# Performance work log

Hardware: AMD Instinct MI355X
Metric: run time of the kernel (lower is better)

Reference implementation:

```python
import jax, jax.numpy as jnp
import numpy as np

D_MODEL = 512; N_HEADS = 8; D_HIDDEN = 512
STACK_DEPTH = 48; STACK_WIDTH = 128; D_FF = 2048; D_SS = 128
SEQ = 512; BATCH = 16
EP = 1e-4; MAX_ITER = 100


def nonsat(x):
    # fixed-point iteration y_ = (2y^3/3 + x)/(y^2+1); torch detaches y each step,
    # so grads flow only through x in the final step. Loop runs on stopped values.
    xs = jax.lax.stop_gradient(x)
    step = lambda y: (2.0 * y ** 3 / 3.0 + xs) / (y * y + 1.0)
    def cond(s):
        y, y_, i = s
        return jnp.logical_and(jnp.mean(jnp.abs(y_ - y)) > EP, i <= MAX_ITER)
    def body(s):
        y, y_, i = s
        return (y_, step(y_), i + 1)
    y_last, _, _ = jax.lax.while_loop(cond, body, (xs, step(xs), jnp.int32(0)))
    return (2.0 * y_last ** 3 / 3.0 + x) / (y_last * y_last + 1.0)


def layer_norm(x, g, b, eps=1e-5):
    m = jnp.mean(x, axis=-1, keepdims=True)
    v = jnp.mean((x - m) ** 2, axis=-1, keepdims=True)
    return (x - m) / jnp.sqrt(v + eps) * g + b


def mha(x, k_mask, wi, bi, wo, bo):
    # x: (S,B,E), torch nn.MultiheadAttention with combined in_proj, causal mask
    S, B, E = x.shape
    H = N_HEADS; hd = E // H
    qkv = x @ wi.T + bi
    q, k, v = jnp.split(qkv, 3, axis=-1)
    to_heads = lambda t: t.reshape(S, B, H, hd).transpose(1, 2, 0, 3)  # (B,H,S,hd)
    q = to_heads(q) * (hd ** -0.5)
    k = to_heads(k); v = to_heads(v)
    scores = jnp.einsum('bhqd,bhkd->bhqk', q, k)
    causal = jnp.triu(jnp.full((S, S), -jnp.inf, dtype=x.dtype), 1)
    scores = scores + causal
    scores = jnp.where(k_mask[:, None, None, :], -jnp.inf, scores)
    a = jax.nn.softmax(scores, axis=-1)
    o = jnp.einsum('bhqk,bhkd->bhqd', a, v).transpose(2, 0, 1, 3).reshape(S, B, E)
    return o @ wo.T + bo


def setup_inputs() -> dict:
    key = jax.random.key(0)
    ks = iter(jax.random.split(key, 32))
    E = D_MODEL
    def w(shape, fan_in):
        return (jax.random.normal(next(ks), shape, jnp.float32) / np.sqrt(fan_in)).astype(jnp.float32)
    inp = {
        'x_in': jax.random.normal(next(ks), (SEQ, BATCH, E), jnp.float32),
        'hidden_prev': jax.random.normal(next(ks), (BATCH, SEQ, D_HIDDEN), jnp.float32),
        'stack_prev': jax.random.normal(next(ks), (BATCH, SEQ, STACK_DEPTH, STACK_WIDTH), jnp.float32),
        'k_mask': jnp.zeros((BATCH, SEQ), dtype=bool),
        'in_proj_w': w((3 * E, E), E), 'in_proj_b': jnp.zeros((3 * E,), jnp.float32),
        'out_proj_w': w((E, E), E), 'out_proj_b': jnp.zeros((E,), jnp.float32),
        'ln1_g': jnp.ones((E,), jnp.float32), 'ln1_b': jnp.zeros((E,), jnp.float32),
        'ln2_g': jnp.ones((E,), jnp.float32), 'ln2_b': jnp.zeros((E,), jnp.float32),
        'ff_w1': w((D_FF, E), E), 'ff_b1': jnp.zeros((D_FF,), jnp.float32),
        'ff_w2': w((E, D_FF), D_FF), 'ff_b2': jnp.zeros((E,), jnp.float32),
        'W_w': w((D_HIDDEN, E), E), 'W_b': jnp.zeros((D_HIDDEN,), jnp.float32),
        'R_w': w((D_HIDDEN, D_HIDDEN), D_HIDDEN), 'R_b': jnp.zeros((D_HIDDEN,), jnp.float32),
        'P_w': w((D_HIDDEN, STACK_WIDTH), STACK_WIDTH), 'P_b': jnp.zeros((D_HIDDEN,), jnp.float32),
        'V_w': w((D_SS, E + D_HIDDEN), E + D_HIDDEN),
        'U_w': w((E, D_SS), D_SS),
        'A_w': w((3, D_HIDDEN), D_HIDDEN), 'A_b': jnp.zeros((3,), jnp.float32),
        'D_w': w((STACK_WIDTH, D_HIDDEN), D_HIDDEN), 'D_b': jnp.zeros((STACK_WIDTH,), jnp.float32),
    }
    return inp


def reference(x_in, hidden_prev, stack_prev, k_mask,
              in_proj_w, in_proj_b, out_proj_w, out_proj_b,
              ln1_g, ln1_b, ln2_g, ln2_b,
              ff_w1, ff_b1, ff_w2, ff_b2,
              W_w, W_b, R_w, R_b, P_w, P_b,
              V_w, U_w, A_w, A_b, D_w, D_b):
    # sublayer 1: pre-norm residual multihead self-attention
    x = x_in + mha(layer_norm(x_in, ln1_g, ln1_b), k_mask,
                   in_proj_w, in_proj_b, out_proj_w, out_proj_b)
    # stack-augmented memory update
    stack_x = stack_prev[:, :, 0, :]                       # (B,S,W) stack top
    xb = x.transpose(1, 0, 2)                              # (B,S,E)
    hidden = xb @ W_w.T + W_b + hidden_prev @ R_w.T + R_b + stack_x @ P_w.T + P_b
    hidden = nonsat(hidden)                                # (B,S,Dh)
    vx = jnp.concatenate([x, hidden.transpose(1, 0, 2)], axis=-1)  # (S,B,E+Dh)
    y = jax.nn.softmax(vx @ V_w.T, axis=-1) @ U_w.T        # (S,B,E)
    x = 0.5 * (x + y)
    stack_inp = nonsat(hidden @ D_w.T + D_b)[:, :, None, :]        # (B,S,1,W)
    controls = jax.nn.softmax(hidden @ A_w.T + A_b, axis=-1)       # (B,S,3)
    a_push = controls[:, :, 0, None, None]
    a_pop = controls[:, :, 1, None, None]
    a_noop = controls[:, :, 2, None, None]
    zeros_bot = jnp.zeros_like(stack_prev[:, :, :1])
    stack_down = jnp.concatenate([stack_prev[:, :, 1:], zeros_bot], axis=2)
    stack_up = jnp.concatenate([stack_inp, stack_prev[:, :, :-1]], axis=2)
    stack = a_noop * stack_prev + a_push * stack_up + a_pop * stack_down
    # sublayer 2: pre-norm residual position-wise FFN
    h = layer_norm(x, ln2_g, ln2_b)
    x = x + (jax.nn.relu(h @ ff_w1.T + ff_b1) @ ff_w2.T + ff_b2)
    return (x, hidden, stack)
```

## Files before the change

### kernel.cpp

```cpp
#include <hip/hip_runtime.h>
#include <stdint.h>

typedef unsigned short u16;
typedef short short8 __attribute__((ext_vector_type(8)));
typedef float f32x4 __attribute__((ext_vector_type(4)));

__device__ __forceinline__ u16 f2b(float f) {
    uint32_t x = __float_as_uint(f);
    uint32_t r = x + 0x7fffu + ((x >> 16) & 1u);
    return (u16)(r >> 16);
}

__device__ __forceinline__ float nonsat_f(float x) {
    float y = x;
#pragma unroll
    for (int t = 0; t < 14; ++t) {
        const float y2 = y * y;
        y = (0.66666667f * y2 * y + x) / (y2 + 1.f);
    }
    return y;
}

__device__ __forceinline__ void gl2lds16(const u16* g, u16* l) {
    __builtin_amdgcn_global_load_lds(
        (const __attribute__((address_space(1))) unsigned int*)g,
        (__attribute__((address_space(3))) unsigned int*)l, 16, 0, 0);
}

template <int MT, int MODE, bool RELU>
__global__ __launch_bounds__(256) void gemm_k(
    const u16* __restrict__ A, int lda,
    const u16* __restrict__ B, int ldb,
    const float* __restrict__ bias,
    int M, int N, int K,
    u16* __restrict__ out_b, float* __restrict__ out_f,
    const float* __restrict__ res_f, u16* __restrict__ out_b2)
{
    constexpr int MI = MT / 64;
    constexpr int WI = MT / 32;
    const int tn = blockIdx.x, tm = blockIdx.y;
    const int tid = threadIdx.x;
    const int wave = tid >> 6, lane = tid & 63;
    const int quad = lane >> 4, mm = lane & 15;
    const int wr = (wave >> 1) * (MT / 2), wc = (wave & 1) * 64;

    __shared__ __align__(16) u16 As[MT * 32];
    __shared__ __align__(16) u16 Bs[128 * 32];

    const f32x4 vzero = {0.f, 0.f, 0.f, 0.f};
    f32x4 acc[WI][4];
#pragma unroll
    for (int i = 0; i < WI; i++)
#pragma unroll
        for (int j = 0; j < 4; j++) acc[i][j] = vzero;

    const int lr = tid >> 2;
    const int lc = (tid & 3) * 8;
    const u16* ag[MI];
#pragma unroll
    for (int h = 0; h < MI; h++)
        ag[h] = A + (size_t)(tm * MT + lr + h * 64) * lda + lc;
    const u16* bg0 = B + (size_t)(tn * 128 + lr) * ldb + lc;
    const u16* bg1 = B + (size_t)(tn * 128 + lr + 64) * ldb + lc;
    u16* asl[MI];
#pragma unroll
    for (int h = 0; h < MI; h++) asl[h] = As + h * 2048 + wave * 512;
    u16* bsl0 = Bs + wave * 512;
    u16* bsl1 = Bs + 2048 + wave * 512;

    for (int kt = 0; kt < K; kt += 32) {
        __syncthreads();
#pragma unroll
        for (int h = 0; h < MI; h++) gl2lds16(ag[h] + kt, asl[h]);
        gl2lds16(bg0 + kt, bsl0);
        gl2lds16(bg1 + kt, bsl1);
        asm volatile("s_waitcnt vmcnt(0)" ::: "memory");
        __syncthreads();
        short8 af[WI], bfr[4];
#pragma unroll
        for (int i = 0; i < WI; i++) af[i] = *(const short8*)(As + (wr + i * 16 + mm) * 32 + quad * 8);
#pragma unroll
        for (int j = 0; j < 4; j++) bfr[j] = *(const short8*)(Bs + (wc + j * 16 + mm) * 32 + quad * 8);
#pragma unroll
        for (int i = 0; i < WI; i++)
#pragma unroll
            for (int j = 0; j < 4; j++)
                acc[i][j] = __builtin_amdgcn_mfma_f32_16x16x32_bf16(af[i], bfr[j], acc[i][j], 0, 0, 0);
    }

#pragma unroll
    for (int j = 0; j < 4; j++) {
        const int colg = tn * 128 + wc + j * 16 + mm;
        const float bv = bias ? bias[colg] : 0.f;
#pragma unroll
        for (int i = 0; i < WI; i++) {
#pragma unroll
            for (int r = 0; r < 4; r++) {
                const int rowg = tm * MT + wr + i * 16 + quad * 4 + r;
                float v = acc[i][j][r] + bv;
                const size_t off = (size_t)rowg * N + colg;
                if constexpr (MODE == 0) {
                    if (RELU) v = fmaxf(v, 0.f);
                    out_b[off] = f2b(v);
                } else if constexpr (MODE == 1) {
                    out_f[off] = v;
                } else if constexpr (MODE == 2) {
                    out_f[off] += v;
                } else if constexpr (MODE == 3) {
                    v += res_f[off];
                    out_f[off] = v;
                    const u16 hb = f2b(v);
                    out_b[off] = hb;
                    out_b2[((size_t)(rowg & 15) * 512 + (rowg >> 4)) * 512 + colg] = hb;
                } else if constexpr (MODE == 4) {
                    v = 0.5f * (v + res_f[off]);
                    out_f[off] = v;
                } else if constexpr (MODE == 5) {
                    v += res_f[off];
                    out_f[off] = v;
                } else if constexpr (MODE == 6) {
                    v = nonsat_f(v + res_f[off]);
                    out_f[off] = v;
                    out_b[off] = f2b(v);
                } else {
                    v = nonsat_f(v);
                    out_f[off] = v;
                }
            }
        }
    }
}

struct CvtArgs {
    const float* s[12];
    unsigned cum[13];
};

__global__ __launch_bounds__(256) void cvt_k(CvtArgs a, u16* __restrict__ arena)
{
    const unsigned t = (blockIdx.x * 256u + threadIdx.x) * 8u;
    if (t >= a.cum[12]) return;
    int g = 0;
#pragma unroll
    for (int i = 1; i < 12; i++)
        if (t >= a.cum[i]) g = i;
    const unsigned e = t - a.cum[g];
    const float* src = (g == 11) ? (a.s[11] + (size_t)(e >> 7) * 6144 + (e & 127))
                                 : (a.s[g] + e);
    float4 u0 = *(const float4*)src;
    float4 u1 = *(const float4*)(src + 4);
    __align__(16) u16 o[8] = {f2b(u0.x), f2b(u0.y), f2b(u0.z), f2b(u0.w),
                              f2b(u1.x), f2b(u1.y), f2b(u1.z), f2b(u1.w)};
    *(int4*)(arena + t) = *(const int4*)o;
}

__global__ __launch_bounds__(64) void attn_k(const u16* __restrict__ QKV, u16* __restrict__ O)
{
    const int qt = blockIdx.x;
    const int bh = blockIdx.y;
    const int b = bh >> 3, h = bh & 7;
    const int lane = threadIdx.x;
    const int quad = lane >> 4, mm = lane & 15;
    const int cbase = h * 64;
    const float NEGINF = -3.0e38f;

    __shared__ __align__(16) u16 Pl[64 * 72];
    __shared__ __align__(16) u16 Vl[64 * 72];

    short8 qf[4][2];
#pragma unroll
    for (int rt = 0; rt < 4; ++rt) {
        const int s = qt * 64 + rt * 16 + mm;
        const u16* p = QKV + ((size_t)s * 16 + b) * 1536 + cbase + quad * 8;
        qf[rt][0] = *(const short8*)(p);
        qf[rt][1] = *(const short8*)(p + 32);
    }

    const f32x4 vzero = {0.f, 0.f, 0.f, 0.f};
    f32x4 of[4][4];
#pragma unroll
    for (int i = 0; i < 4; i++)
#pragma unroll
        for (int j = 0; j < 4; j++) of[i][j] = vzero;
    float mrow[4][4], lrow[4][4];
#pragma unroll
    for (int i = 0; i < 4; i++)
#pragma unroll
        for (int r = 0; r < 4; r++) { mrow[i][r] = NEGINF; lrow[i][r] = 0.f; }

    for (int kt = 0; kt <= qt; ++kt) {
        short8 kf[4][2];
#pragma unroll
        for (int nt = 0; nt < 4; ++nt) {
            const int kk = kt * 64 + nt * 16 + mm;
            const u16* p = QKV + ((size_t)kk * 16 + b) * 1536 + 512 + cbase + quad * 8;
            kf[nt][0] = *(const short8*)(p);
            kf[nt][1] = *(const short8*)(p + 32);
        }
        f32x4 sf[4][4];
#pragma unroll
        for (int i = 0; i < 4; i++)
#pragma unroll
            for (int j = 0; j < 4; j++) sf[i][j] = vzero;
#pragma unroll
        for (int i = 0; i < 4; i++)
#pragma unroll
            for (int j = 0; j < 4; j++) {
                sf[i][j] = __builtin_amdgcn_mfma_f32_16x16x32_bf16(qf[i][0], kf[j][0], sf[i][j], 0, 0, 0);
                sf[i][j] = __builtin_amdgcn_mfma_f32_16x16x32_bf16(qf[i][1], kf[j][1], sf[i][j], 0, 0, 0);
            }
        {
            const int kk = lane >> 3, c8 = (lane & 7) * 8;
#pragma unroll
            for (int it = 0; it < 8; ++it) {
                const int key = kt * 64 + it * 8 + kk;
                int4 v = *(const int4*)(QKV + ((size_t)key * 16 + b) * 1536 + 1024 + cbase + c8);
                *(int4*)(Vl + (it * 8 + kk) * 72 + c8) = v;
            }
        }
        const bool diag = (kt == qt);
#pragma unroll
        for (int i = 0; i < 4; i++)
#pragma unroll
            for (int j = 0; j < 4; j++)
#pragma unroll
                for (int r = 0; r < 4; r++) {
                    float v = sf[i][j][r] * 0.125f;
                    if (diag) {
                        const int q = i * 16 + quad * 4 + r;
                        const int k = j * 16 + mm;
                        if (k > q) v = NEGINF;
                    }
                    sf[i][j][r] = v;
                }
#pragma unroll
        for (int i = 0; i < 4; i++) {
#pragma unroll
            for (int r = 0; r < 4; r++) {
                float mx = fmaxf(fmaxf(sf[i][0][r], sf[i][1][r]), fmaxf(sf[i][2][r], sf[i][3][r]));
                mx = fmaxf(mx, __shfl_xor(mx, 1));
                mx = fmaxf(mx, __shfl_xor(mx, 2));
                mx = fmaxf(mx, __shfl_xor(mx, 4));
                mx = fmaxf(mx, __shfl_xor(mx, 8));
                const float mnew = fmaxf(mrow[i][r], mx);
                const float alpha = __expf(mrow[i][r] - mnew);
                mrow[i][r] = mnew;
                float psum = 0.f;
#pragma unroll
                for (int j = 0; j < 4; j++) {
                    float p = __expf(sf[i][j][r] - mnew);
                    sf[i][j][r] = p;
                    psum += p;
                }
                psum += __shfl_xor(psum, 1);
                psum += __shfl_xor(psum, 2);
                psum += __shfl_xor(psum, 4);
                psum += __shfl_xor(psum, 8);
                lrow[i][r] = lrow[i][r] * alpha + psum;
#pragma unroll
                for (int j = 0; j < 4; j++) of[i][j][r] *= alpha;
            }
        }
#pragma unroll
        for (int i = 0; i < 4; i++)
#pragma unroll
            for (int j = 0; j < 4; j++)
#pragma unroll
                for (int r = 0; r < 4; r++)
                    Pl[(i * 16 + quad * 4 + r) * 72 + j * 16 + mm] = f2b(sf[i][j][r]);
        __syncthreads();
        short8 pa[4][2];
#pragma unroll
        for (int i = 0; i < 4; i++) {
            pa[i][0] = *(const short8*)(Pl + (i * 16 + mm) * 72 + quad * 8);
            pa[i][1] = *(const short8*)(Pl + (i * 16 + mm) * 72 + 32 + quad * 8);
        }
#pragma unroll
        for (int j = 0; j < 4; j++) {
#pragma unroll
            for (int kc = 0; kc < 2; ++kc) {
                short8 vb;
#pragma unroll
                for (int e = 0; e < 8; e++)
                    vb[e] = (short)Vl[(kc * 32 + quad * 8 + e) * 72 + j * 16 + mm];
#pragma unroll
                for (int i = 0; i < 4; i++)
                    of[i][j] = __builtin_amdgcn_mfma_f32_16x16x32_bf16(pa[i][kc], vb, of[i][j], 0, 0, 0);
            }
        }
        __syncthreads();
    }
#pragma unroll
    for (int i = 0; i < 4; i++)
#pragma unroll
        for (int r = 0; r < 4; r++) {
            const int s = qt * 64 + i * 16 + quad * 4 + r;
            const float inv = 1.f / lrow[i][r];
#pragma unroll
            for (int j = 0; j < 4; j++)
                O[((size_t)s * 16 + b) * 512 + cbase + j * 16 + mm] = f2b(of[i][j][r] * inv);
        }
}

__global__ __launch_bounds__(256) void ln_k(const float* __restrict__ x,
                                            const float* __restrict__ g,
                                            const float* __restrict__ be,
                                            u16* __restrict__ out)
{
    const int row = blockIdx.x * 4 + (threadIdx.x >> 6);
    const int lane = threadIdx.x & 63;
    const float* p = x + (size_t)row * 512 + lane * 8;
    float4 u0 = *(const float4*)p;
    float4 u1 = *(const float4*)(p + 4);
    float v[8] = {u0.x, u0.y, u0.z, u0.w, u1.x, u1.y, u1.z, u1.w};
    float s = 0.f, s2 = 0.f;
#pragma unroll
    for (int j = 0; j < 8; j++) { s += v[j]; s2 += v[j] * v[j]; }
#pragma unroll
    for (int off = 1; off < 64; off <<= 1) { s += __shfl_xor(s, off); s2 += __shfl_xor(s2, off); }
    const float mean = s * (1.f / 512.f);
    const float var = s2 * (1.f / 512.f) - mean * mean;
    const float rstd = rsqrtf(fmaxf(var, 0.f) + 1e-5f);
    float4 g0 = *(const float4*)(g + lane * 8);
    float4 g1 = *(const float4*)(g + lane * 8 + 4);
    float4 b0 = *(const float4*)(be + lane * 8);
    float4 b1 = *(const float4*)(be + lane * 8 + 4);
    const float gg[8] = {g0.x, g0.y, g0.z, g0.w, g1.x, g1.y, g1.z, g1.w};
    const float bb[8] = {b0.x, b0.y, b0.z, b0.w, b1.x, b1.y, b1.z, b1.w};
    __align__(16) u16 o[8];
#pragma unroll
    for (int j = 0; j < 8; j++)
        o[j] = f2b((v[j] - mean) * rstd * gg[j] + bb[j]);
    *(int4*)(out + (size_t)row * 512 + lane * 8) = *(const int4*)o;
}

__global__ __launch_bounds__(128) void vxpack_k(const u16* __restrict__ Xb, const u16* __restrict__ Hb,
                                                u16* __restrict__ VX)
{
    const int r = blockIdx.x;
    const int lane = threadIdx.x;
    const int s = r >> 4, b = r & 15;
    if (lane < 64) {
        *(int4*)(VX + (size_t)r * 1024 + lane * 8) =
            *(const int4*)(Xb + (size_t)r * 512 + lane * 8);
    } else {
        const int l = lane - 64;
        *(int4*)(VX + (size_t)r * 1024 + 512 + l * 8) =
            *(const int4*)(Hb + ((size_t)b * 512 + s) * 512 + l * 8);
    }
}

__global__ __launch_bounds__(256) void softmax128_k(const float* __restrict__ in, u16* __restrict__ out)
{
    const int row = blockIdx.x * 4 + (threadIdx.x >> 6);
    const int lane = threadIdx.x & 63;
    const float* p = in + (size_t)row * 128;
    const float a = p[lane], b = p[lane + 64];
    float mx = fmaxf(a, b);
#pragma unroll
    for (int off = 1; off < 64; off <<= 1) mx = fmaxf(mx, __shfl_xor(mx, off));
    const float ea = __expf(a - mx), eb = __expf(b - mx);
    float s = ea + eb;
#pragma unroll
    for (int off = 1; off < 64; off <<= 1) s += __shfl_xor(s, off);
    const float inv = 1.f / s;
    out[(size_t)row * 128 + lane] = f2b(ea * inv);
    out[(size_t)row * 128 + 64 + lane] = f2b(eb * inv);
}

__global__ __launch_bounds__(256) void controls_k(const float* __restrict__ H, const float* __restrict__ Aw,
                                                  const float* __restrict__ Ab, float* __restrict__ ctrl)
{
    const int row = blockIdx.x * 4 + (threadIdx.x >> 6);
    const int lane = threadIdx.x & 63;
    const float* hp = H + (size_t)row * 512 + lane * 8;
    float4 h0 = *(const float4*)hp;
    float4 h1 = *(const float4*)(hp + 4);
    const float hv[8] = {h0.x, h0.y, h0.z, h0.w, h1.x, h1.y, h1.z, h1.w};
    float d[3];
#pragma unroll
    for (int w = 0; w < 3; ++w) {
        const float* ap = Aw + w * 512 + lane * 8;
        float4 a0 = *(const float4*)ap;
        float4 a1 = *(const float4*)(ap + 4);
        const float av[8] = {a0.x, a0.y, a0.z, a0.w, a1.x, a1.y, a1.z, a1.w};
        float acc = 0.f;
#pragma unroll
        for (int j = 0; j < 8; j++) acc += hv[j] * av[j];
        d[w] = acc;
    }
#pragma unroll
    for (int off = 1; off < 64; off <<= 1) {
        d[0] += __shfl_xor(d[0], off);
        d[1] += __shfl_xor(d[1], off);
        d[2] += __shfl_xor(d[2], off);
    }
    const float l0 = d[0] + Ab[0], l1 = d[1] + Ab[1], l2 = d[2] + Ab[2];
    const float mx = fmaxf(l0, fmaxf(l1, l2));
    const float e0 = __expf(l0 - mx), e1 = __expf(l1 - mx), e2 = __expf(l2 - mx);
    const float inv = 1.f / (e0 + e1 + e2);
    if (lane == 0) {
        ctrl[(size_t)row * 3 + 0] = e0 * inv;
        ctrl[(size_t)row * 3 + 1] = e1 * inv;
        ctrl[(size_t)row * 3 + 2] = e2 * inv;
    }
}

__global__ __launch_bounds__(256) void stack_k(const float* __restrict__ sp_all, const float* __restrict__ sin,
                                               const float* __restrict__ ctrl, float* __restrict__ out)
{
    const int bs = blockIdx.x;
    const int t = blockIdx.y * 256 + threadIdx.x;
    const int d = t >> 4;
    const int w = (t & 15) * 8;
    const float* sp = sp_all + (size_t)bs * 6144;
    const float pu = ctrl[(size_t)bs * 3 + 0];
    const float po = ctrl[(size_t)bs * 3 + 1];
    const float no = ctrl[(size_t)bs * 3 + 2];
    float cur[8], up[8], dn[8];
    {
        const float* p = sp + d * 128 + w;
        float4 c0 = *(const float4*)p, c1 = *(const float4*)(p + 4);
        cur[0]=c0.x; cur[1]=c0.y; cur[2]=c0.z; cur[3]=c0.w; cur[4]=c1.x; cur[5]=c1.y; cur[6]=c1.z; cur[7]=c1.w;
    }
    {
        const float* p = (d == 0) ? (sin + (size_t)bs * 128 + w) : (sp + (d - 1) * 128 + w);
        float4 c0 = *(const float4*)p, c1 = *(const float4*)(p + 4);
        up[0]=c0.x; up[1]=c0.y; up[2]=c0.z; up[3]=c0.w; up[4]=c1.x; up[5]=c1.y; up[6]=c1.z; up[7]=c1.w;
    }
    if (d < 47) {
        const float* p = sp + (d + 1) * 128 + w;
        float4 c0 = *(const float4*)p, c1 = *(const float4*)(p + 4);
        dn[0]=c0.x; dn[1]=c0.y; dn[2]=c0.z; dn[3]=c0.w; dn[4]=c1.x; dn[5]=c1.y; dn[6]=c1.z; dn[7]=c1.w;
    } else {
#pragma unroll
        for (int j = 0; j < 8; j++) dn[j] = 0.f;
    }
    float o[8];
#pragma unroll
    for (int j = 0; j < 8; j++)
        o[j] = no * cur[j] + pu * up[j] + po * dn[j];
    float* q = out + (size_t)bs * 6144 + d * 128 + w;
    *(float4*)q = make_float4(o[0], o[1], o[2], o[3]);
    *(float4*)(q + 4) = make_float4(o[4], o[5], o[6], o[7]);
}

static constexpr size_t O_A1 = 0;
static constexpr size_t O_QKV = O_A1 + 8388608;
static constexpr size_t O_OATT = O_QKV + 25165824;
static constexpr size_t O_X1F = O_OATT + 8388608;
static constexpr size_t O_HPF = O_X1F + 16777216;
static constexpr size_t O_VL = O_HPF + 16777216;
static constexpr size_t O_X2F = O_VL + 4194304;
static constexpr size_t O_H2 = O_X2F + 16777216;
static constexpr size_t WS_NEED = O_H2 + 8388608;
static constexpr size_t O_XB = O_QKV;
static constexpr size_t O_VX = O_QKV;
static constexpr size_t O_PS = O_QKV + 16777216;
static constexpr size_t O_SIN = O_QKV + 18874368;
static constexpr size_t O_CTRL = O_QKV + 23068672;
static constexpr size_t O_X1B = O_A1;
static constexpr size_t O_FF1 = O_X1F;
static constexpr size_t O_HB = O_H2;

static constexpr unsigned C_INPJ = 0;
static constexpr unsigned C_OUTP = 786432;
static constexpr unsigned C_FF1W = 1048576;
static constexpr unsigned C_FF2W = 2097152;
static constexpr unsigned C_WW   = 3145728;
static constexpr unsigned C_RW   = 3407872;
static constexpr unsigned C_PW   = 3670016;
static constexpr unsigned C_VW   = 3735552;
static constexpr unsigned C_UW   = 3866624;
static constexpr unsigned C_DW   = 3932160;
static constexpr unsigned C_HPB  = 3997696;
static constexpr unsigned C_SXB  = 8192000;
static constexpr unsigned C_TOT  = 9240576;
static constexpr size_t ARENA_OFF_IN_STACK = 201326592 - (size_t)C_TOT * 2;

extern "C" void kernel_launch(void* const* d_in, const int* in_sizes, int n_in,
                              void* d_out, int out_size, void* d_ws, size_t ws_size,
                              hipStream_t stream)
{
    (void)in_sizes; (void)n_in; (void)out_size;
    if (ws_size < WS_NEED) return;

    const float* x_in        = (const float*)d_in[0];
    const float* hidden_prev = (const float*)d_in[1];
    const float* stack_prev  = (const float*)d_in[2];
    const float* in_proj_w   = (const float*)d_in[4];
    const float* in_proj_b   = (const float*)d_in[5];
    const float* out_proj_w  = (const float*)d_in[6];
    const float* out_proj_b  = (const float*)d_in[7];
    const float* ln1_g       = (const float*)d_in[8];
    const float* ln1_b       = (const float*)d_in[9];
    const float* ln2_g       = (const float*)d_in[10];
    const float* ln2_b       = (const float*)d_in[11];
    const float* ff_w1       = (const float*)d_in[12];
    const float* ff_b1       = (const float*)d_in[13];
    const float* ff_w2       = (const float*)d_in[14];
    const float* ff_b2       = (const float*)d_in[15];
    const float* W_w         = (const float*)d_in[16];
    const float* W_b         = (const float*)d_in[17];
    const float* R_w         = (const float*)d_in[18];
    const float* R_b         = (const float*)d_in[19];
    const float* P_w         = (const float*)d_in[20];
    const float* P_b         = (const float*)d_in[21];
    const float* V_w         = (const float*)d_in[22];
    const float* U_w         = (const float*)d_in[23];
    const float* A_w         = (const float*)d_in[24];
    const float* A_b         = (const float*)d_in[25];
    const float* D_w         = (const float*)d_in[26];
    const float* D_b         = (const float*)d_in[27];

    char* ws = (char*)d_ws;
    u16* A1   = (u16*)(ws + O_A1);
    u16* QKV  = (u16*)(ws + O_QKV);
    u16* OATT = (u16*)(ws + O_OATT);
    float* X1F = (float*)(ws + O_X1F);
    float* HPF = (float*)(ws + O_HPF);
    float* VL  = (float*)(ws + O_VL);
    float* X2F = (float*)(ws + O_X2F);
    u16* H2   = (u16*)(ws + O_H2);
    u16* HB   = (u16*)(ws + O_HB);
    u16* VX   = (u16*)(ws + O_VX);
    u16* PS   = (u16*)(ws + O_PS);
    float* SIN = (float*)(ws + O_SIN);
    float* CTRL = (float*)(ws + O_CTRL);
    u16* XB   = (u16*)(ws + O_XB);
    u16* X1B  = (u16*)(ws + O_X1B);
    u16* FF1  = (u16*)(ws + O_FF1);

    float* out = (float*)d_out;
    float* x_out = out;
    float* hid_out = out + 4194304;
    float* stack_out = out + 8388608;
    u16* arena = (u16*)((char*)stack_out + ARENA_OFF_IN_STACK);

    CvtArgs ca;
    ca.s[0] = in_proj_w; ca.s[1] = out_proj_w; ca.s[2] = ff_w1; ca.s[3] = ff_w2;
    ca.s[4] = W_w; ca.s[5] = R_w; ca.s[6] = P_w; ca.s[7] = V_w;
    ca.s[8] = U_w; ca.s[9] = D_w; ca.s[10] = hidden_prev; ca.s[11] = stack_prev;
    const unsigned cums[13] = {C_INPJ, C_OUTP, C_FF1W, C_FF2W, C_WW, C_RW, C_PW,
                               C_VW, C_UW, C_DW, C_HPB, C_SXB, C_TOT};
    for (int i = 0; i < 13; i++) ca.cum[i] = cums[i];
    cvt_k<<<4512, 256, 0, stream>>>(ca, arena);

    ln_k<<<2048, 256, 0, stream>>>(x_in, ln1_g, ln1_b, A1);
    gemm_k<128, 0, false><<<dim3(12, 64), 256, 0, stream>>>(
        A1, 512, arena + C_INPJ, 512, in_proj_b, 8192, 1536, 512, QKV, nullptr, nullptr, nullptr);
    attn_k<<<dim3(8, 128), 64, 0, stream>>>(QKV, OATT);
    gemm_k<64, 3, false><<<dim3(4, 128), 256, 0, stream>>>(
        OATT, 512, arena + C_OUTP, 512, out_proj_b, 8192, 512, 512, X1B, X1F, x_in, XB);
    gemm_k<64, 1, false><<<dim3(4, 128), 256, 0, stream>>>(
        XB, 512, arena + C_WW, 512, W_b, 8192, 512, 512, nullptr, HPF, nullptr, nullptr);
    gemm_k<64, 2, false><<<dim3(4, 128), 256, 0, stream>>>(
        arena + C_HPB, 512, arena + C_RW, 512, R_b, 8192, 512, 512, nullptr, HPF, nullptr, nullptr);
    gemm_k<64, 6, false><<<dim3(4, 128), 256, 0, stream>>>(
        arena + C_SXB, 128, arena + C_PW, 128, P_b, 8192, 512, 128, HB, hid_out, HPF, nullptr);
    vxpack_k<<<8192, 128, 0, stream>>>(X1B, HB, VX);
    gemm_k<64, 1, false><<<dim3(1, 128), 256, 0, stream>>>(
        VX, 1024, arena + C_VW, 1024, nullptr, 8192, 128, 1024, nullptr, VL, nullptr, nullptr);
    softmax128_k<<<2048, 256, 0, stream>>>(VL, PS);
    gemm_k<64, 4, false><<<dim3(4, 128), 256, 0, stream>>>(
        PS, 128, arena + C_UW, 128, nullptr, 8192, 512, 128, nullptr, X2F, X1F, nullptr);
    gemm_k<64, 7, false><<<dim3(1, 128), 256, 0, stream>>>(
        HB, 512, arena + C_DW, 512, D_b, 8192, 128, 512, nullptr, SIN, nullptr, nullptr);
    controls_k<<<2048, 256, 0, stream>>>(hid_out, A_w, A_b, CTRL);
    ln_k<<<2048, 256, 0, stream>>>(X2F, ln2_g, ln2_b, H2);
    gemm_k<128, 0, true><<<dim3(16, 64), 256, 0, stream>>>(
        H2, 512, arena + C_FF1W, 512, ff_b1, 8192, 2048, 512, FF1, nullptr, nullptr, nullptr);
    gemm_k<64, 5, false><<<dim3(4, 128), 256, 0, stream>>>(
        FF1, 2048, arena + C_FF2W, 2048, ff_b2, 8192, 512, 2048, nullptr, x_out, X2F, nullptr);
    stack_k<<<dim3(8192, 3), 256, 0, stream>>>(stack_prev, SIN, CTRL, stack_out);
}
```

Measured before the change: 769.7 us.

## Fuse hidden projections into one K-concatenated GEMM and fold softmax into V GEMM

The three hidden-state projections (W, R, P) are merged into a single GEMM over a concatenated K=1152 operand. Their biases are pre-summed and the weights and activations are packed into matching layouts during the conversion kernel. The out-projection and hidden epilogues now write straight into the VX concat buffer, which removes the vxpack kernel, and the 128-wide softmax is fused into the V GEMM epilogue via LDS. This drops several launches and the fp32 HPF read-modify-write round trips. The cost is more complex indexing and scattered epilogue stores.

```diff
diff --git a/kernel.cpp b/kernel.cpp
--- a/kernel.cpp
+++ b/kernel.cpp
@@ -88,6 +88,36 @@
                 acc[i][j] = __builtin_amdgcn_mfma_f32_16x16x32_bf16(af[i], bfr[j], acc[i][j], 0, 0, 0);
     }
 
+    if constexpr (MODE == 8) {
+        __shared__ __align__(16) float Sm[64 * 130];
+#pragma unroll
+        for (int j = 0; j < 4; j++)
+#pragma unroll
+            for (int i = 0; i < WI; i++)
+#pragma unroll
+                for (int r = 0; r < 4; r++)
+                    Sm[(wr + i * 16 + quad * 4 + r) * 130 + wc + j * 16 + mm] = acc[i][j][r];
+        __syncthreads();
+#pragma unroll
+        for (int rr = 0; rr < 16; ++rr) {
+            const int row_l = wave * 16 + rr;
+            const float a = Sm[row_l * 130 + lane];
+            const float b = Sm[row_l * 130 + 64 + lane];
+            float mx = fmaxf(a, b);
+#pragma unroll
+            for (int off = 1; off < 64; off <<= 1) mx = fmaxf(mx, __shfl_xor(mx, off));
+            const float ea = __expf(a - mx), eb = __expf(b - mx);
+            float s = ea + eb;
+#pragma unroll
+            for (int off = 1; off < 64; off <<= 1) s += __shfl_xor(s, off);
+            const float inv = 1.f / s;
+            const size_t rowg = (size_t)tm * MT + row_l;
+            out_b[rowg * 128 + lane] = f2b(ea * inv);
+            out_b[rowg * 128 + 64 + lane] = f2b(eb * inv);
+        }
+        return;
+    }
+
 #pragma unroll
     for (int j = 0; j < 4; j++) {
         const int colg = tn * 128 + wc + j * 16 + mm;
@@ -102,16 +132,12 @@
                 if constexpr (MODE == 0) {
                     if (RELU) v = fmaxf(v, 0.f);
                     out_b[off] = f2b(v);
-                } else if constexpr (MODE == 1) {
-                    out_f[off] = v;
-                } else if constexpr (MODE == 2) {
-                    out_f[off] += v;
                 } else if constexpr (MODE == 3) {
                     v += res_f[off];
                     out_f[off] = v;
                     const u16 hb = f2b(v);
-                    out_b[off] = hb;
-                    out_b2[((size_t)(rowg & 15) * 512 + (rowg >> 4)) * 512 + colg] = hb;
+                    out_b[(size_t)rowg * 1024 + colg] = hb;
+                    out_b2[((size_t)(rowg & 15) * 512 + (rowg >> 4)) * 1152 + colg] = hb;
                 } else if constexpr (MODE == 4) {
                     v = 0.5f * (v + res_f[off]);
                     out_f[off] = v;
@@ -119,9 +145,9 @@
                     v += res_f[off];
                     out_f[off] = v;
                 } else if constexpr (MODE == 6) {
-                    v = nonsat_f(v + res_f[off]);
+                    v = nonsat_f(v);
                     out_f[off] = v;
-                    out_b[off] = f2b(v);
+                    out_b[((size_t)(rowg & 511) * 16 + (rowg >> 9)) * 1024 + 512 + colg] = f2b(v);
                 } else {
                     v = nonsat_f(v);
                     out_f[off] = v;
@@ -136,8 +162,29 @@
     unsigned cum[13];
 };
 
-__global__ __launch_bounds__(256) void cvt_k(CvtArgs a, u16* __restrict__ arena)
-{
+static constexpr unsigned C_INPJ = 0;
+static constexpr unsigned C_OUTP = 786432;
+static constexpr unsigned C_FF1W = 1048576;
+static constexpr unsigned C_FF2W = 2097152;
+static constexpr unsigned C_WRP  = 3145728;
+static constexpr unsigned C_VW   = 3735552;
+static constexpr unsigned C_UW   = 3866624;
+static constexpr unsigned C_DW   = 3932160;
+static constexpr unsigned C_WTOT = 3997696;
+static constexpr unsigned C_TOTAL = 9240576;
+
+__global__ __launch_bounds__(256) void cvt_k(CvtArgs a, u16* __restrict__ wa, u16* __restrict__ ha,
+                                             const float* __restrict__ Wb, const float* __restrict__ Rb,
+                                             const float* __restrict__ Pb, float* __restrict__ bsum)
+{
+    if (blockIdx.x == gridDim.x - 1) {
+        if (threadIdx.x < 128) {
+            const int c = threadIdx.x * 4;
+#pragma unroll
+            for (int k = 0; k < 4; k++) bsum[c + k] = Wb[c + k] + Rb[c + k] + Pb[c + k];
+        }
+        return;
+    }
     const unsigned t = (blockIdx.x * 256u + threadIdx.x) * 8u;
     if (t >= a.cum[12]) return;
     int g = 0;
@@ -145,13 +192,32 @@
     for (int i = 1; i < 12; i++)
         if (t >= a.cum[i]) g = i;
     const unsigned e = t - a.cum[g];
-    const float* src = (g == 11) ? (a.s[11] + (size_t)(e >> 7) * 6144 + (e & 127))
-                                 : (a.s[g] + e);
+    const float* src;
+    u16* dst;
+    if (g == 10) {
+        src = a.s[10] + e;
+        dst = ha + (size_t)(e >> 9) * 1152 + 512 + (e & 511);
+    } else if (g == 11) {
+        src = a.s[11] + (size_t)(e >> 7) * 6144 + (e & 127);
+        dst = ha + (size_t)(e >> 7) * 1152 + 1024 + (e & 127);
+    } else if (g == 4) {
+        src = a.s[4] + e;
+        dst = wa + C_WRP + (size_t)(e >> 9) * 1152 + (e & 511);
+    } else if (g == 5) {
+        src = a.s[5] + e;
+        dst = wa + C_WRP + (size_t)(e >> 9) * 1152 + 512 + (e & 511);
+    } else if (g == 6) {
+        src = a.s[6] + e;
+        dst = wa + C_WRP + (size_t)(e >> 7) * 1152 + 1024 + (e & 127);
+    } else {
+        src = a.s[g] + e;
+        dst = wa + t;
+    }
     float4 u0 = *(const float4*)src;
     float4 u1 = *(const float4*)(src + 4);
     __align__(16) u16 o[8] = {f2b(u0.x), f2b(u0.y), f2b(u0.z), f2b(u0.w),
                               f2b(u1.x), f2b(u1.y), f2b(u1.z), f2b(u1.w)};
-    *(int4*)(arena + t) = *(const int4*)o;
+    *(int4*)dst = *(const int4*)o;
 }
 
 __global__ __launch_bounds__(64) void attn_k(const u16* __restrict__ QKV, u16* __restrict__ O)
@@ -332,40 +398,6 @@
     for (int j = 0; j < 8; j++)
         o[j] = f2b((v[j] - mean) * rstd * gg[j] + bb[j]);
     *(int4*)(out + (size_t)row * 512 + lane * 8) = *(const int4*)o;
-}
-
-__global__ __launch_bounds__(128) void vxpack_k(const u16* __restrict__ Xb, const u16* __restrict__ Hb,
-                                                u16* __restrict__ VX)
-{
-    const int r = blockIdx.x;
-    const int lane = threadIdx.x;
-    const int s = r >> 4, b = r & 15;
-    if (lane < 64) {
-        *(int4*)(VX + (size_t)r * 1024 + lane * 8) =
-            *(const int4*)(Xb + (size_t)r * 512 + lane * 8);
-    } else {
-        const int l = lane - 64;
-        *(int4*)(VX + (size_t)r * 1024 + 512 + l * 8) =
-            *(const int4*)(Hb + ((size_t)b * 512 + s) * 512 + l * 8);
-    }
-}
-
-__global__ __launch_bounds__(256) void softmax128_k(const float* __restrict__ in, u16* __restrict__ out)
-{
-    const int row = blockIdx.x * 4 + (threadIdx.x >> 6);
-    const int lane = threadIdx.x & 63;
-    const float* p = in + (size_t)row * 128;
-    const float a = p[lane], b = p[lane + 64];
-    float mx = fmaxf(a, b);
-#pragma unroll
-    for (int off = 1; off < 64; off <<= 1) mx = fmaxf(mx, __shfl_xor(mx, off));
-    const float ea = __expf(a - mx), eb = __expf(b - mx);
-    float s = ea + eb;
-#pragma unroll
-    for (int off = 1; off < 64; off <<= 1) s += __shfl_xor(s, off);
-    const float inv = 1.f / s;
-    out[(size_t)row * 128 + lane] = f2b(ea * inv);
-    out[(size_t)row * 128 + 64 + lane] = f2b(eb * inv);
 }
 
 __global__ __launch_bounds__(256) void controls_k(const float* __restrict__ H, const float* __restrict__ Aw,
@@ -424,7 +456,8 @@
         cur[0]=c0.x; cur[1]=c0.y; cur[2]=c0.z; cur[3]=c0.w; cur[4]=c1.x; cur[5]=c1.y; cur[6]=c1.z; cur[7]=c1.w;
     }
     {
-        const float* p = (d == 0) ? (sin + (size_t)bs * 128 + w) : (sp + (d - 1) * 128 + w);
+        const int bb = bs >> 9, ss = bs & 511;
+        const float* p = (d == 0) ? (sin + ((size_t)ss * 16 + bb) * 128 + w) : (sp + (d - 1) * 128 + w);
         float4 c0 = *(const float4*)p, c1 = *(const float4*)(p + 4);
         up[0]=c0.x; up[1]=c0.y; up[2]=c0.z; up[3]=c0.w; up[4]=c1.x; up[5]=c1.y; up[6]=c1.z; up[7]=c1.w;
     }
@@ -454,29 +487,16 @@
 static constexpr size_t O_X2F = O_VL + 4194304;
 static constexpr size_t O_H2 = O_X2F + 16777216;
 static constexpr size_t WS_NEED = O_H2 + 8388608;
-static constexpr size_t O_XB = O_QKV;
 static constexpr size_t O_VX = O_QKV;
 static constexpr size_t O_PS = O_QKV + 16777216;
 static constexpr size_t O_SIN = O_QKV + 18874368;
 static constexpr size_t O_CTRL = O_QKV + 23068672;
-static constexpr size_t O_X1B = O_A1;
 static constexpr size_t O_FF1 = O_X1F;
-static constexpr size_t O_HB = O_H2;
-
-static constexpr unsigned C_INPJ = 0;
-static constexpr unsigned C_OUTP = 786432;
-static constexpr unsigned C_FF1W = 1048576;
-static constexpr unsigned C_FF2W = 2097152;
-static constexpr unsigned C_WW   = 3145728;
-static constexpr unsigned C_RW   = 3407872;
-static constexpr unsigned C_PW   = 3670016;
-static constexpr unsigned C_VW   = 3735552;
-static constexpr unsigned C_UW   = 3866624;
-static constexpr unsigned C_DW   = 3932160;
-static constexpr unsigned C_HPB  = 3997696;
-static constexpr unsigned C_SXB  = 8192000;
-static constexpr unsigned C_TOT  = 9240576;
-static constexpr size_t ARENA_OFF_IN_STACK = 201326592 - (size_t)C_TOT * 2;
+
+static constexpr size_t WA_BYTES = (size_t)C_WTOT * 2;
+static constexpr size_t HA_BYTES = (size_t)8192 * 1152 * 2;
+static constexpr size_t STASH_BYTES = WA_BYTES + HA_BYTES;
+static constexpr size_t STASH_OFF = 201326592 - STASH_BYTES;
 
 extern "C" void kernel_launch(void* const* d_in, const int* in_sizes, int n_in,
                               void* d_out, int out_size, void* d_ws, size_t ws_size,
@@ -518,59 +538,50 @@
     u16* QKV  = (u16*)(ws + O_QKV);
     u16* OATT = (u16*)(ws + O_OATT);
     float* X1F = (float*)(ws + O_X1F);
-    float* HPF = (float*)(ws + O_HPF);
-    float* VL  = (float*)(ws + O_VL);
+    float* bsum = (float*)(ws + O_VL);
     float* X2F = (float*)(ws + O_X2F);
     u16* H2   = (u16*)(ws + O_H2);
-    u16* HB   = (u16*)(ws + O_HB);
     u16* VX   = (u16*)(ws + O_VX);
     u16* PS   = (u16*)(ws + O_PS);
     float* SIN = (float*)(ws + O_SIN);
     float* CTRL = (float*)(ws + O_CTRL);
-    u16* XB   = (u16*)(ws + O_XB);
-    u16* X1B  = (u16*)(ws + O_X1B);
     u16* FF1  = (u16*)(ws + O_FF1);
 
     float* out = (float*)d_out;
     float* x_out = out;
     float* hid_out = out + 4194304;
     float* stack_out = out + 8388608;
-    u16* arena = (u16*)((char*)stack_out + ARENA_OFF_IN_STACK);
+    u16* wa = (u16*)((char*)stack_out + STASH_OFF);
+    u16* ha = (u16*)((char*)wa + WA_BYTES);
 
     CvtArgs ca;
     ca.s[0] = in_proj_w; ca.s[1] = out_proj_w; ca.s[2] = ff_w1; ca.s[3] = ff_w2;
     ca.s[4] = W_w; ca.s[5] = R_w; ca.s[6] = P_w; ca.s[7] = V_w;
     ca.s[8] = U_w; ca.s[9] = D_w; ca.s[10] = hidden_prev; ca.s[11] = stack_prev;
-    const unsigned cums[13] = {C_INPJ, C_OUTP, C_FF1W, C_FF2W, C_WW, C_RW, C_PW,
-                               C_VW, C_UW, C_DW, C_HPB, C_SXB, C_TOT};
+    const unsigned cums[13] = {C_INPJ, C_OUTP, C_FF1W, C_FF2W, 3145728, 3407872, 3670016,
+                               C_VW, C_UW, C_DW, C_WTOT, 8192000, C_TOTAL};
     for (int i = 0; i < 13; i++) ca.cum[i] = cums[i];
-    cvt_k<<<4512, 256, 0, stream>>>(ca, arena);
+    cvt_k<<<4513, 256, 0, stream>>>(ca, wa, ha, W_b, R_b, P_b, bsum);
 
     ln_k<<<2048, 256, 0, stream>>>(x_in, ln1_g, ln1_b, A1);
     gemm_k<128, 0, false><<<dim3(12, 64), 256, 0, stream>>>(
-        A1, 512, arena + C_INPJ, 512, in_proj_b, 8192, 1536, 512, QKV, nullptr, nullptr, nullptr);
+        A1, 512, wa + C_INPJ, 512, in_proj_b, 8192, 1536, 512, QKV, nullptr, nullptr, nullptr);
     attn_k<<<dim3(8, 128), 64, 0, stream>>>(QKV, OATT);
     gemm_k<64, 3, false><<<dim3(4, 128), 256, 0, stream>>>(
-        OATT, 512, arena + C_OUTP, 512, out_proj_b, 8192, 512, 512, X1B, X1F, x_in, XB);
-    gemm_k<64, 1, false><<<dim3(4, 128), 256, 0, stream>>>(
-        XB, 512, arena + C_WW, 512, W_b, 8192, 512, 512, nullptr, HPF, nullptr, nullptr);
-    gemm_k<64, 2, false><<<dim3(4, 128), 256, 0, stream>>>(
-        arena + C_HPB, 512, arena + C_RW, 512, R_b, 8192, 512, 512, nullptr, HPF, nullptr, nullptr);
+        OATT, 512, wa + C_OUTP, 512, out_proj_b, 8192, 512, 512, VX, X1F, x_in, ha);
     gemm_k<64, 6, false><<<dim3(4, 128), 256, 0, stream>>>(
-        arena + C_SXB, 128, arena + C_PW, 128, P_b, 8192, 512, 128, HB, hid_out, HPF, nullptr);
-    vxpack_k<<<8192, 128, 0, stream>>>(X1B, HB, VX);
-    gemm_k<64, 1, false><<<dim3(1, 128), 256, 0, stream>>>(
-        VX, 1024, arena + C_VW, 1024, nullptr, 8192, 128, 1024, nullptr, VL, nullptr, nullptr);
-    softmax128_k<<<2048, 256, 0, stream>>>(VL, PS);
+        ha, 1152, wa + C_WRP, 1152, bsum, 8192, 512, 1152, VX, hid_out, nullptr, nullptr);
+    gemm_k<64, 8, false><<<dim3(1, 128), 256, 0, stream>>>(
+        VX, 1024, wa + C_VW, 1024, nullptr, 8192, 128, 1024, PS, nullptr, nullptr, nullptr);
     gemm_k<64, 4, false><<<dim3(4, 128), 256, 0, stream>>>(
-        PS, 128, arena + C_UW, 128, nullptr, 8192, 512, 128, nullptr, X2F, X1F, nullptr);
+        PS, 128, wa + C_UW, 128, nullptr, 8192, 512, 128, nullptr, X2F, X1F, nullptr);
     gemm_k<64, 7, false><<<dim3(1, 128), 256, 0, stream>>>(
-        HB, 512, arena + C_DW, 512, D_b, 8192, 128, 512, nullptr, SIN, nullptr, nullptr);
+        VX + 512, 1024, wa + C_DW, 512, D_b, 8192, 128, 512, nullptr, SIN, nullptr, nullptr);
     controls_k<<<2048, 256, 0, stream>>>(hid_out, A_w, A_b, CTRL);
     ln_k<<<2048, 256, 0, stream>>>(X2F, ln2_g, ln2_b, H2);
     gemm_k<128, 0, true><<<dim3(16, 64), 256, 0, stream>>>(
-        H2, 512, arena + C_FF1W, 512, ff_b1, 8192, 2048, 512, FF1, nullptr, nullptr, nullptr);
+        H2, 512, wa + C_FF1W, 512, ff_b1, 8192, 2048, 512, FF1, nullptr, nullptr, nullptr);
     gemm_k<64, 5, false><<<dim3(4, 128), 256, 0, stream>>>(
-        FF1, 2048, arena + C_FF2W, 2048, ff_b2, 8192, 512, 2048, nullptr, x_out, X2F, nullptr);
+        FF1, 2048, wa + C_FF2W, 2048, ff_b2, 8192, 512, 2048, nullptr, x_out, X2F, nullptr);
     stack_k<<<dim3(8192, 3), 256, 0, stream>>>(stack_prev, SIN, CTRL, stack_out);
 }
```

After: 735.4 us. 1.05x faster.
